# Kernel optimization log

Hardware: AMD Instinct MI355X
Metric: run time of the kernel (lower is better)

## Reference

```python
import jax, jax.numpy as jnp
import numpy as np

B, N, FIN, FOUT = 8, 2048, 128, 64
ALPHA = 0.2      # LeakyReLU negative slope
NEG_INF = -9e15  # matches torch constant -9000000000000000.0
LN_EPS = 1e-5


def setup_inputs() -> dict:
    key = jax.random.key(0)
    k1, k2, k3, k4 = jax.random.split(key, 4)
    x = jax.random.normal(k1, (B, N, FIN), dtype=jnp.float32)
    adj = jax.random.randint(k2, (B, N, N), 0, 2, dtype=jnp.int32)
    # params: W is nn.Linear(in,out,bias=False) -> stored here as [FIN,FOUT];
    # a is nn.Linear(2*out,1,bias=False) -> vector of length 2*FOUT.
    W = jax.random.normal(k3, (FIN, FOUT), dtype=jnp.float32) * (1.0 / np.sqrt(FIN))
    a = jax.random.normal(k4, (2 * FOUT,), dtype=jnp.float32) * (1.0 / np.sqrt(2 * FOUT))
    gamma = jnp.ones((FOUT,), dtype=jnp.float32)
    beta = jnp.zeros((FOUT,), dtype=jnp.float32)
    return {"x": x, "adj": adj, "W": W, "a": a, "gamma": gamma, "beta": beta}


def reference(x, adj, W, a, gamma, beta):
    h = jnp.einsum('bnf,fo->bno', x, W)                      # [B,N,FOUT]
    fout = h.shape[-1]
    a1, a2 = a[:fout], a[fout:]
    # a·cat(h_i,h_j) == h_i·a1 + h_j·a2 -> avoid O(N^2*2F) concat tensor
    s1 = h @ a1                                              # [B,N]
    s2 = h @ a2                                              # [B,N]
    e = jax.nn.leaky_relu(s1[:, :, None] + s2[:, None, :], ALPHA)  # [B,N,N]
    att = jnp.where(adj > 0, e, NEG_INF)
    att = jax.nn.softmax(att, axis=2)
    h_prime = jnp.einsum('bij,bjf->bif', att, h)             # [B,N,FOUT]
    # LayerNorm over last dim
    mu = jnp.mean(h_prime, axis=-1, keepdims=True)
    var = jnp.mean((h_prime - mu) ** 2, axis=-1, keepdims=True)
    y = (h_prime - mu) * jax.lax.rsqrt(var + LN_EPS) * gamma + beta
    return jax.nn.elu(y)
```

## Files before the change

### kernel.cpp

```cpp
#include <hip/hip_runtime.h>
#include <hip/hip_bf16.h>

#define B_    8
#define N_    2048
#define FIN_  128
#define FOUT_ 64
#define ALPHA_ 0.2f
#define LN_EPS_ 1e-5f

typedef __attribute__((ext_vector_type(8))) short short8;
typedef __attribute__((ext_vector_type(4))) float f32x4;

__device__ __forceinline__ short f2bf(float f) {
    __hip_bfloat16 h = __float2bfloat16(f);
    return *reinterpret_cast<short*>(&h);
}
__device__ __forceinline__ float bf2f(short s) {
    return __uint_as_float(((unsigned)(unsigned short)s) << 16);
}

__global__ __launch_bounds__(256) void k_proj(
    const float* __restrict__ x,
    const float* __restrict__ W,
    const float* __restrict__ a,
    unsigned short* __restrict__ hT,
    float* __restrict__ s1, float* __restrict__ s2)
{
    __shared__ short Wb[16 * 64 * 8];
    __shared__ float Wa1l[FIN_], Wa2l[FIN_];

    const int t = threadIdx.x;
    const int row0 = blockIdx.x * 64;
    const int b   = row0 >> 11;
    const int ib0 = row0 & (N_ - 1);

    #pragma unroll
    for (int c = 0; c < 4; ++c) {
        int g = t + 256 * c;
        int u = g >> 6, ln = g & 63;
        int ks = u >> 2, nt = u & 3;
        int n  = nt * 16 + (ln & 15);
        int k0 = ks * 32 + (ln >> 4) * 8;
        short8 v;
        #pragma unroll
        for (int jj = 0; jj < 8; ++jj) v[jj] = f2bf(W[(k0 + jj) * FOUT_ + n]);
        *(short8*)&Wb[g * 8] = v;
    }
    if (t < FIN_) {
        float a1 = 0.f, a2 = 0.f;
        #pragma unroll
        for (int n = 0; n < FOUT_; n += 4) {
            float4 wv  = *(const float4*)&W[t * FOUT_ + n];
            float4 av1 = *(const float4*)&a[n];
            float4 av2 = *(const float4*)&a[FOUT_ + n];
            a1 += wv.x * av1.x + wv.y * av1.y + wv.z * av1.z + wv.w * av1.w;
            a2 += wv.x * av2.x + wv.y * av2.y + wv.z * av2.z + wv.w * av2.w;
        }
        Wa1l[t] = a1; Wa2l[t] = a2;
    }
    __syncthreads();

    const int wave = t >> 6, lane = t & 63;
    const int m = lane & 15, quad = lane >> 4;
    const int row = row0 + wave * 16 + m;

    short8 fa[4];
    float s1p = 0.f, s2p = 0.f;
    #pragma unroll
    for (int ks = 0; ks < 4; ++ks) {
        int k0 = ks * 32 + quad * 8;
        float4 x0 = *(const float4*)&x[(size_t)row * FIN_ + k0];
        float4 x1 = *(const float4*)&x[(size_t)row * FIN_ + k0 + 4];
        float xs[8] = {x0.x, x0.y, x0.z, x0.w, x1.x, x1.y, x1.z, x1.w};
        short8 v;
        #pragma unroll
        for (int jj = 0; jj < 8; ++jj) {
            v[jj] = f2bf(xs[jj]);
            s1p += xs[jj] * Wa1l[k0 + jj];
            s2p += xs[jj] * Wa2l[k0 + jj];
        }
        fa[ks] = v;
    }
    s1p += __shfl_xor(s1p, 16); s1p += __shfl_xor(s1p, 32);
    s2p += __shfl_xor(s2p, 16); s2p += __shfl_xor(s2p, 32);
    if (lane < 16) {
        s1[row0 + wave * 16 + lane] = s1p;
        s2[row0 + wave * 16 + lane] = s2p;
    }

    f32x4 acc[4];
    #pragma unroll
    for (int nt = 0; nt < 4; ++nt) acc[nt] = (f32x4){0.f, 0.f, 0.f, 0.f};
    #pragma unroll
    for (int ks = 0; ks < 4; ++ks) {
        #pragma unroll
        for (int nt = 0; nt < 4; ++nt) {
            short8 fb = *(short8*)&Wb[((ks * 4 + nt) * 64 + lane) * 8];
            acc[nt] = __builtin_amdgcn_mfma_f32_16x16x32_bf16(fa[ks], fb, acc[nt], 0, 0, 0);
        }
    }
    #pragma unroll
    for (int nt = 0; nt < 4; ++nt) {
        int o  = nt * 16 + m;
        int ib = ib0 + wave * 16 + quad * 4;
        ushort4 hv;
        hv.x = (unsigned short)f2bf(acc[nt][0]);
        hv.y = (unsigned short)f2bf(acc[nt][1]);
        hv.z = (unsigned short)f2bf(acc[nt][2]);
        hv.w = (unsigned short)f2bf(acc[nt][3]);
        *(ushort4*)&hT[(size_t)(b * 64 + o) * N_ + ib] = hv;
    }
}

__global__ __launch_bounds__(256) void k_attn(
    const int* __restrict__ adj,
    const unsigned short* __restrict__ hT,
    const float* __restrict__ s1g, const float* __restrict__ s2g,
    const float* __restrict__ gamma, const float* __restrict__ beta,
    float* __restrict__ out)
{
    __shared__ short Hb[16 * 64 * 8];
    __shared__ short Wf[4 * 64 * 8];
    __shared__ float s2l[128];
    __shared__ float s1l[16], ml[16];
    __shared__ float lp[4][16];
    __shared__ float hp[16 * 64];
    __shared__ float red[4];

    const int t = threadIdx.x;
    const int wave = t >> 6, lane = t & 63;
    const int i_ = lane & 15, quad = lane >> 4;
    const int b  = blockIdx.x >> 7;
    const int i0 = (blockIdx.x & 127) * 16;
    const size_t sbase  = (size_t)b * N_;
    const size_t hTbase = (size_t)b * 64 * N_;

    float mx = -3.0e38f;
    #pragma unroll
    for (int k = 0; k < 8; ++k) mx = fmaxf(mx, s2g[sbase + t + 256 * k]);
    #pragma unroll
    for (int d = 32; d; d >>= 1) mx = fmaxf(mx, __shfl_xor(mx, d));
    if (lane == 0) red[wave] = mx;
    __syncthreads();
    {
        float smax = fmaxf(fmaxf(red[0], red[1]), fmaxf(red[2], red[3]));
        if (t < 16) {
            float s1v = s1g[sbase + i0 + t];
            s1l[t] = s1v;
            float v = s1v + smax;
            ml[t] = fmaxf(v, ALPHA_ * v);
        }
    }

    f32x4 acc = (f32x4){0.f, 0.f, 0.f, 0.f};
    float lpart = 0.f;

    for (int j0 = 0; j0 < N_; j0 += 128) {
        __syncthreads();
        #pragma unroll
        for (int c = 0; c < 4; ++c) {
            int g = t + 256 * c;
            int u = g >> 6, ln = g & 63;
            int ks = u >> 2, nt = u & 3;
            int o  = nt * 16 + (ln & 15);
            int jr = ks * 32 + (ln >> 4) * 8;
            short8 v = *(const short8*)&hT[hTbase + (size_t)o * N_ + j0 + jr];
            *(short8*)&Hb[g * 8] = v;
        }
        if (t < 128) s2l[t] = s2g[sbase + j0 + t];
        __syncthreads();

        {
            int jr = wave * 32 + quad * 8;
            const int* ap = &adj[(sbase + i0 + i_) * N_ + j0 + jr];
            int4 a0 = *(const int4*)ap;
            int4 a1 = *(const int4*)(ap + 4);
            int am[8] = {a0.x, a0.y, a0.z, a0.w, a1.x, a1.y, a1.z, a1.w};
            float s1v = s1l[i_], mv = ml[i_];
            float sum = 0.f;
            short8 wv;
            #pragma unroll
            for (int jj = 0; jj < 8; ++jj) {
                float ev = s1v + s2l[jr + jj];
                ev = fmaxf(ev, ALPHA_ * ev);
                float w = (am[jj] > 0) ? __expf(ev - mv) : 0.f;
                short ws = f2bf(w);
                wv[jj] = ws;
                sum += bf2f(ws);
            }
            *(short8*)&Wf[t * 8] = wv;
            lpart += sum;
        }
        __syncthreads();

        #pragma unroll
        for (int ks = 0; ks < 4; ++ks) {
            short8 fa = *(short8*)&Wf[(ks * 64 + lane) * 8];
            short8 fb = *(short8*)&Hb[((ks * 4 + wave) * 64 + lane) * 8];
            acc = __builtin_amdgcn_mfma_f32_16x16x32_bf16(fa, fb, acc, 0, 0, 0);
        }
    }

    lpart += __shfl_xor(lpart, 16);
    lpart += __shfl_xor(lpart, 32);
    if (lane < 16) lp[wave][lane] = lpart;
    __syncthreads();

    {
        int col = wave * 16 + i_;
        #pragma unroll
        for (int reg = 0; reg < 4; ++reg) {
            int r = quad * 4 + reg;
            float l = lp[0][r] + lp[1][r] + lp[2][r] + lp[3][r];
            hp[r * 64 + col] = acc[reg] / l;
        }
    }
    __syncthreads();

    {
        int o = lane;
        float g  = gamma[o];
        float be = beta[o];
        #pragma unroll
        for (int rr = 0; rr < 4; ++rr) {
            int i = wave * 4 + rr;
            float v = hp[i * 64 + o];
            float mu = v;
            #pragma unroll
            for (int d = 32; d; d >>= 1) mu += __shfl_xor(mu, d);
            mu *= (1.f / 64.f);
            float dv = v - mu;
            float var = dv * dv;
            #pragma unroll
            for (int d = 32; d; d >>= 1) var += __shfl_xor(var, d);
            var *= (1.f / 64.f);
            float y = dv * rsqrtf(var + LN_EPS_) * g + be;
            out[(sbase + i0 + i) * FOUT_ + o] = y > 0.f ? y : __expf(y) - 1.f;
        }
    }
}

extern "C" void kernel_launch(void* const* d_in, const int* in_sizes, int n_in,
                              void* d_out, int out_size, void* d_ws, size_t ws_size,
                              hipStream_t stream) {
    const float* x     = (const float*)d_in[0];
    const int*   adj   = (const int*)d_in[1];
    const float* W     = (const float*)d_in[2];
    const float* a     = (const float*)d_in[3];
    const float* gamma = (const float*)d_in[4];
    const float* beta  = (const float*)d_in[5];
    float* out = (float*)d_out;

    unsigned short* hT = (unsigned short*)d_ws;
    float* s1 = (float*)((char*)d_ws + (size_t)B_ * 64 * N_ * 2);
    float* s2 = s1 + (size_t)B_ * N_;

    k_proj<<<256, 256, 0, stream>>>(x, W, a, hT, s1, s2);
    k_attn<<<B_ * (N_ / 16), 256, 0, stream>>>(adj, hT, s1, s2, gamma, beta, out);
}
```

Measured before the change: 226.4 us.

## Prefetch adj and hT tiles in registers, preload s2, split weight prep kernel

The attention kernel now issues the global loads for the next adjacency chunk and the current hT tile into registers before the exp/weight computation, and stores hT to LDS afterwards. This lets global latency overlap compute and removes one barrier per tile. The full s2 row is staged in LDS once, and the Wf/hp buffers share one LDS pool. The projection is split into a one-block prep kernel that converts W to bf16 and computes W·a once, plus a proj kernel with twice as many smaller blocks. The cost is an extra launch, more LDS (an 8KB s2 buffer), and a hand-written barrier in inline asm.

```diff
diff --git a/kernel.cpp b/kernel.cpp
--- a/kernel.cpp
+++ b/kernel.cpp
@@ -19,21 +19,11 @@
     return __uint_as_float(((unsigned)(unsigned short)s) << 16);
 }
 
-__global__ __launch_bounds__(256) void k_proj(
-    const float* __restrict__ x,
-    const float* __restrict__ W,
-    const float* __restrict__ a,
-    unsigned short* __restrict__ hT,
-    float* __restrict__ s1, float* __restrict__ s2)
+__global__ __launch_bounds__(256) void k_prep(
+    const float* __restrict__ W, const float* __restrict__ a,
+    short* __restrict__ Wbf, float* __restrict__ Wa1g, float* __restrict__ Wa2g)
 {
-    __shared__ short Wb[16 * 64 * 8];
-    __shared__ float Wa1l[FIN_], Wa2l[FIN_];
-
     const int t = threadIdx.x;
-    const int row0 = blockIdx.x * 64;
-    const int b   = row0 >> 11;
-    const int ib0 = row0 & (N_ - 1);
-
     #pragma unroll
     for (int c = 0; c < 4; ++c) {
         int g = t + 256 * c;
@@ -44,7 +34,7 @@
         short8 v;
         #pragma unroll
         for (int jj = 0; jj < 8; ++jj) v[jj] = f2bf(W[(k0 + jj) * FOUT_ + n]);
-        *(short8*)&Wb[g * 8] = v;
+        *(short8*)&Wbf[g * 8] = v;
     }
     if (t < FIN_) {
         float a1 = 0.f, a2 = 0.f;
@@ -56,13 +46,30 @@
             a1 += wv.x * av1.x + wv.y * av1.y + wv.z * av1.z + wv.w * av1.w;
             a2 += wv.x * av2.x + wv.y * av2.y + wv.z * av2.z + wv.w * av2.w;
         }
-        Wa1l[t] = a1; Wa2l[t] = a2;
-    }
+        Wa1g[t] = a1; Wa2g[t] = a2;
+    }
+}
+
+__global__ __launch_bounds__(256) void k_proj(
+    const float* __restrict__ x,
+    const short* __restrict__ Wbf,
+    const float* __restrict__ Wa1g, const float* __restrict__ Wa2g,
+    unsigned short* __restrict__ hT,
+    float* __restrict__ s1, float* __restrict__ s2)
+{
+    __shared__ float Wa1l[FIN_], Wa2l[FIN_];
+    const int t = threadIdx.x;
+    const int row0 = blockIdx.x * 32;
+    const int b   = row0 >> 11;
+    const int ib0 = row0 & (N_ - 1);
+
+    if (t < FIN_) { Wa1l[t] = Wa1g[t]; Wa2l[t] = Wa2g[t]; }
     __syncthreads();
 
     const int wave = t >> 6, lane = t & 63;
     const int m = lane & 15, quad = lane >> 4;
-    const int row = row0 + wave * 16 + m;
+    const int mt = wave & 1, nt0 = (wave >> 1) * 2;
+    const int row = row0 + mt * 16 + m;
 
     short8 fa[4];
     float s1p = 0.f, s2p = 0.f;
@@ -83,31 +90,31 @@
     }
     s1p += __shfl_xor(s1p, 16); s1p += __shfl_xor(s1p, 32);
     s2p += __shfl_xor(s2p, 16); s2p += __shfl_xor(s2p, 32);
-    if (lane < 16) {
+    if (wave < 2 && lane < 16) {
         s1[row0 + wave * 16 + lane] = s1p;
         s2[row0 + wave * 16 + lane] = s2p;
     }
 
-    f32x4 acc[4];
-    #pragma unroll
-    for (int nt = 0; nt < 4; ++nt) acc[nt] = (f32x4){0.f, 0.f, 0.f, 0.f};
+    f32x4 acc[2];
+    acc[0] = (f32x4){0.f, 0.f, 0.f, 0.f};
+    acc[1] = (f32x4){0.f, 0.f, 0.f, 0.f};
     #pragma unroll
     for (int ks = 0; ks < 4; ++ks) {
         #pragma unroll
-        for (int nt = 0; nt < 4; ++nt) {
-            short8 fb = *(short8*)&Wb[((ks * 4 + nt) * 64 + lane) * 8];
-            acc[nt] = __builtin_amdgcn_mfma_f32_16x16x32_bf16(fa[ks], fb, acc[nt], 0, 0, 0);
-        }
-    }
-    #pragma unroll
-    for (int nt = 0; nt < 4; ++nt) {
-        int o  = nt * 16 + m;
-        int ib = ib0 + wave * 16 + quad * 4;
+        for (int q = 0; q < 2; ++q) {
+            short8 fb = *(const short8*)&Wbf[((ks * 4 + nt0 + q) * 64 + lane) * 8];
+            acc[q] = __builtin_amdgcn_mfma_f32_16x16x32_bf16(fa[ks], fb, acc[q], 0, 0, 0);
+        }
+    }
+    #pragma unroll
+    for (int q = 0; q < 2; ++q) {
+        int o  = (nt0 + q) * 16 + m;
+        int ib = ib0 + mt * 16 + quad * 4;
         ushort4 hv;
-        hv.x = (unsigned short)f2bf(acc[nt][0]);
-        hv.y = (unsigned short)f2bf(acc[nt][1]);
-        hv.z = (unsigned short)f2bf(acc[nt][2]);
-        hv.w = (unsigned short)f2bf(acc[nt][3]);
+        hv.x = (unsigned short)f2bf(acc[q][0]);
+        hv.y = (unsigned short)f2bf(acc[q][1]);
+        hv.z = (unsigned short)f2bf(acc[q][2]);
+        hv.w = (unsigned short)f2bf(acc[q][3]);
         *(ushort4*)&hT[(size_t)(b * 64 + o) * N_ + ib] = hv;
     }
 }
@@ -120,12 +127,13 @@
     float* __restrict__ out)
 {
     __shared__ short Hb[16 * 64 * 8];
-    __shared__ short Wf[4 * 64 * 8];
-    __shared__ float s2l[128];
+    __shared__ __align__(16) char pool[4096];
+    __shared__ float s2l[N_];
     __shared__ float s1l[16], ml[16];
     __shared__ float lp[4][16];
-    __shared__ float hp[16 * 64];
     __shared__ float red[4];
+    short* Wf = (short*)pool;
+    float* hp = (float*)pool;
 
     const int t = threadIdx.x;
     const int wave = t >> 6, lane = t & 63;
@@ -135,9 +143,12 @@
     const size_t sbase  = (size_t)b * N_;
     const size_t hTbase = (size_t)b * 64 * N_;
 
-    float mx = -3.0e38f;
-    #pragma unroll
-    for (int k = 0; k < 8; ++k) mx = fmaxf(mx, s2g[sbase + t + 256 * k]);
+    float4 v0 = *(const float4*)&s2g[sbase + 4 * t];
+    float4 v1 = *(const float4*)&s2g[sbase + 4 * (t + 256)];
+    *(float4*)&s2l[4 * t] = v0;
+    *(float4*)&s2l[4 * (t + 256)] = v1;
+    float mx = fmaxf(fmaxf(fmaxf(v0.x, v0.y), fmaxf(v0.z, v0.w)),
+                     fmaxf(fmaxf(v1.x, v1.y), fmaxf(v1.z, v1.w)));
     #pragma unroll
     for (int d = 32; d; d >>= 1) mx = fmaxf(mx, __shfl_xor(mx, d));
     if (lane == 0) red[wave] = mx;
@@ -152,36 +163,37 @@
         }
     }
 
+    const int jr = wave * 32 + quad * 8;
+    const int* adjrow = &adj[(sbase + i0 + i_) * N_ + jr];
+
+    int4 pa0 = *(const int4*)&adjrow[0];
+    int4 pa1 = *(const int4*)&adjrow[4];
+
     f32x4 acc = (f32x4){0.f, 0.f, 0.f, 0.f};
     float lpart = 0.f;
 
-    for (int j0 = 0; j0 < N_; j0 += 128) {
-        __syncthreads();
+    for (int tile = 0; tile < 16; ++tile) {
+        const int j0 = tile * 128;
+        asm volatile("s_waitcnt lgkmcnt(0)\n\ts_barrier" ::: "memory");
+
+        short8 hv[4];
         #pragma unroll
         for (int c = 0; c < 4; ++c) {
-            int g = t + 256 * c;
-            int u = g >> 6, ln = g & 63;
+            int u  = c * 4 + wave;
             int ks = u >> 2, nt = u & 3;
-            int o  = nt * 16 + (ln & 15);
-            int jr = ks * 32 + (ln >> 4) * 8;
-            short8 v = *(const short8*)&hT[hTbase + (size_t)o * N_ + j0 + jr];
-            *(short8*)&Hb[g * 8] = v;
-        }
-        if (t < 128) s2l[t] = s2g[sbase + j0 + t];
-        __syncthreads();
+            int o  = nt * 16 + i_;
+            int j2 = ks * 32 + quad * 8;
+            hv[c] = *(const short8*)&hT[hTbase + (size_t)o * N_ + j0 + j2];
+        }
 
         {
-            int jr = wave * 32 + quad * 8;
-            const int* ap = &adj[(sbase + i0 + i_) * N_ + j0 + jr];
-            int4 a0 = *(const int4*)ap;
-            int4 a1 = *(const int4*)(ap + 4);
-            int am[8] = {a0.x, a0.y, a0.z, a0.w, a1.x, a1.y, a1.z, a1.w};
+            int am[8] = {pa0.x, pa0.y, pa0.z, pa0.w, pa1.x, pa1.y, pa1.z, pa1.w};
             float s1v = s1l[i_], mv = ml[i_];
             float sum = 0.f;
             short8 wv;
             #pragma unroll
             for (int jj = 0; jj < 8; ++jj) {
-                float ev = s1v + s2l[jr + jj];
+                float ev = s1v + s2l[j0 + jr + jj];
                 ev = fmaxf(ev, ALPHA_ * ev);
                 float w = (am[jj] > 0) ? __expf(ev - mv) : 0.f;
                 short ws = f2bf(w);
@@ -191,6 +203,17 @@
             *(short8*)&Wf[t * 8] = wv;
             lpart += sum;
         }
+
+        {
+            int j0n = (j0 + 128) & (N_ - 1);
+            pa0 = *(const int4*)&adjrow[j0n];
+            pa1 = *(const int4*)&adjrow[j0n + 4];
+        }
+
+        #pragma unroll
+        for (int c = 0; c < 4; ++c)
+            *(short8*)&Hb[((c * 4 + wave) * 64 + lane) * 8] = hv[c];
+
         __syncthreads();
 
         #pragma unroll
@@ -251,10 +274,15 @@
     const float* beta  = (const float*)d_in[5];
     float* out = (float*)d_out;
 
-    unsigned short* hT = (unsigned short*)d_ws;
-    float* s1 = (float*)((char*)d_ws + (size_t)B_ * 64 * N_ * 2);
-    float* s2 = s1 + (size_t)B_ * N_;
-
-    k_proj<<<256, 256, 0, stream>>>(x, W, a, hT, s1, s2);
+    char* ws = (char*)d_ws;
+    unsigned short* hT = (unsigned short*)ws;
+    float* s1   = (float*)(ws + (size_t)B_ * 64 * N_ * 2);
+    float* s2   = s1 + (size_t)B_ * N_;
+    short* Wbf  = (short*)(s2 + (size_t)B_ * N_);
+    float* Wa1g = (float*)(Wbf + 16 * 64 * 8);
+    float* Wa2g = Wa1g + FIN_;
+
+    k_prep<<<1, 256, 0, stream>>>(W, a, Wbf, Wa1g, Wa2g);
+    k_proj<<<512, 256, 0, stream>>>(x, Wbf, Wa1g, Wa2g, hT, s1, s2);
     k_attn<<<B_ * (N_ / 16), 256, 0, stream>>>(adj, hT, s1, s2, gamma, beta, out);
 }
```

After: 219.8 us. 2.9% less time.
